# Kernel tuning notes

Measured on AMD Instinct MI355X. Metric: run time of the kernel, lower is better.

Reference implementation:

```python
import jax, jax.numpy as jnp
import numpy as np
from jax import lax

B, N = 2, 8192
H = W = 256
KNN_K = 33          # includes self, as in _computeDensity
RADIUS = 0.1
CUTOFF = 1.0        # cutOffThreshold: a dx^2 + b dy^2 + c dx dy <= cutoffC
WIN = 9             # fixed splat footprint (ellipse extents ~1-3 px, clamped at 15 in source)
EPS = 1e-8


def setup_inputs() -> dict:
    key = jax.random.key(0)
    k1, k2, k3, k4, k5 = jax.random.split(key, 5)
    points = jax.random.normal(k1, (B, N, 3), jnp.float32)
    # projected pixel coordinates, kept a few px inside the image
    proj_xy = jax.random.uniform(k2, (B, N, 2), jnp.float32, 4.0, W - 4.0)
    # ellipse coefficients a, b, c with 4ab - c^2 > 0 (valid ellipse)
    ab = jax.random.uniform(k3, (B, N, 2), jnp.float32, 0.1, 0.5)
    c = jax.random.uniform(k4, (B, N, 1), jnp.float32, -0.05, 0.05)
    ellipse_params = jnp.concatenate([ab, c], axis=-1)
    colors = jax.random.uniform(k5, (B, N, 3), jnp.float32)
    return {"points": points, "proj_xy": proj_xy,
            "ellipse_params": ellipse_params, "colors": colors}


def _compute_density(points):
    # faithful jax version of _computeDensity: KNN gaussian density
    r2 = RADIUS * RADIUS
    sq = jnp.sum(points * points, axis=-1)                      # [B,N]
    # pairwise squared distances [B,N,N]
    d2 = sq[:, :, None] + sq[:, None, :] - 2.0 * jnp.einsum('bnd,bmd->bnm', points, points)
    neg_d2k, _ = lax.top_k(-d2, KNN_K)                          # k nearest (incl. self)
    d2k = jnp.maximum(-neg_d2k[:, :, 1:], 0.0)                  # drop self, [B,N,K-1]
    w = jnp.exp(-d2k / r2 / 4.0)
    w = jnp.where(d2k > r2, 0.0, w)
    return jnp.sum(w, axis=-1)                                  # [B,N]


def reference(points, proj_xy, ellipse_params, colors):
    density = _compute_density(points)                          # [B,N]
    a = ellipse_params[..., 0]
    b = ellipse_params[..., 1]
    c = ellipse_params[..., 2]
    x = proj_xy[..., 0]
    y = proj_xy[..., 1]
    # _findEllipseBoundingBox extents, clamped at 15 as in the grad path
    den = 4.0 * a * b - c * c
    xE = jnp.minimum(jnp.sqrt(4.0 * b * CUTOFF / den), 15.0)    # [B,N]
    yE = jnp.minimum(jnp.sqrt(4.0 * a * CUTOFF / den), 15.0)

    # fixed WINxWIN footprint around floor(proj) (jit-friendly bbox)
    R = WIN // 2
    offs = jnp.arange(-R, R + 1, dtype=jnp.float32)
    ox, oy = jnp.meshgrid(offs, offs, indexing='ij')
    ox = ox.reshape(-1)                                         # [P]
    oy = oy.reshape(-1)
    x0 = jnp.floor(x)
    y0 = jnp.floor(y)
    px = x0[..., None] + ox                                     # [B,N,P]
    py = y0[..., None] + oy
    dx = px - x[..., None]
    dy = py - y[..., None]
    # elliptical gaussian splat weight, truncated at cutoff
    Q = a[..., None] * dx * dx + b[..., None] * dy * dy + c[..., None] * dx * dy
    inb = (px >= 0) & (px < W) & (py >= 0) & (py < H)
    bbox = (jnp.abs(dx) <= xE[..., None] + 1.0) & (jnp.abs(dy) <= yE[..., None] + 1.0)
    mask = inb & bbox & (Q <= CUTOFF)
    w = jnp.where(mask, jnp.exp(-0.5 * Q) * density[..., None], 0.0)  # [B,N,P]

    # scatter-accumulate weighted colors and weights per pixel
    pxi = jnp.clip(px.astype(jnp.int32), 0, W - 1)
    pyi = jnp.clip(py.astype(jnp.int32), 0, H - 1)
    bi = jnp.arange(B, dtype=jnp.int32)[:, None, None]
    flat = ((bi * H + pyi) * W + pxi).reshape(-1)               # [B*N*P]
    wc = (w[..., None] * colors[:, :, None, :]).reshape(-1, 3)
    wf = w.reshape(-1)
    img_c = jnp.zeros((B * H * W, 3), jnp.float32).at[flat].add(wc)
    img_w = jnp.zeros((B * H * W,), jnp.float32).at[flat].add(wf)
    image = img_c / (img_w[:, None] + EPS)
    return image.reshape(B, H, W, 3)
```

## Files before the change

### kernel.cpp

```cpp
#include <hip/hip_runtime.h>

#define NB  2
#define NP  8192
#define IMH 256
#define IMW 256
#define NBKT 1024

constexpr float R2F = 0.01f;
constexpr float BK_SCALE = 64.f;
constexpr float BK_OFF   = 8.f;
#define BK_PAD 7

__device__ __forceinline__ int bucket_of(float x) {
    int b = (int)floorf((x + BK_OFF) * BK_SCALE);
    return min(max(b, 0), NBKT - 1);
}

__global__ __launch_bounds__(1024) void binsort_kernel(
    const float* __restrict__ pts, float4* __restrict__ sorted,
    int* __restrict__ sidx, int* __restrict__ offsets)
{
    __shared__ int cntA[NBKT], cntB[NBKT], cur[NBKT];
    const int b   = blockIdx.x;
    const int tid = threadIdx.x;
    const float* __restrict__ base = pts + (size_t)b * NP * 3;

    cntA[tid] = 0;
    __syncthreads();

    float xs[8], ys[8], zs[8]; int bks[8];
    #pragma unroll
    for (int k = 0; k < 8; ++k) {
        const int i = k * 1024 + tid;
        xs[k] = base[i * 3 + 0];
        ys[k] = base[i * 3 + 1];
        zs[k] = base[i * 3 + 2];
        bks[k] = bucket_of(xs[k]);
        atomicAdd(&cntA[bks[k]], 1);
    }
    __syncthreads();

    int* src = cntA; int* dst = cntB;
    for (int off = 1; off < NBKT; off <<= 1) {
        int v = src[tid];
        if (tid >= off) v += src[tid - off];
        dst[tid] = v;
        __syncthreads();
        int* tmp = src; src = dst; dst = tmp;
    }
    const int start = (tid == 0) ? 0 : src[tid - 1];
    offsets[b * (NBKT + 1) + tid] = start;
    if (tid == 0) offsets[b * (NBKT + 1) + NBKT] = NP;
    cur[tid] = start;
    __syncthreads();

    #pragma unroll
    for (int k = 0; k < 8; ++k) {
        const int i = k * 1024 + tid;
        const int slot = atomicAdd(&cur[bks[k]], 1);
        const float sq = __fadd_rn(__fadd_rn(__fmul_rn(xs[k], xs[k]),
                                             __fmul_rn(ys[k], ys[k])),
                                   __fmul_rn(zs[k], zs[k]));
        sorted[(size_t)b * NP + slot] = make_float4(xs[k], ys[k], zs[k], sq);
        sidx  [(size_t)b * NP + slot] = i;
    }
}

__global__ __launch_bounds__(256) void density_kernel(
    const float4* __restrict__ sorted, const int* __restrict__ sidx,
    const int* __restrict__ offsets, float* __restrict__ density)
{
    const int wave = threadIdx.x >> 6, lane = threadIdx.x & 63;
    const int w  = blockIdx.x * 4 + wave;
    const int s0 = w * 8;
    const int b  = s0 >> 13;
    const int sb = s0 & (NP - 1);
    const float4* __restrict__ sp = sorted + (size_t)b * NP;

    float xi[8], yi[8], zi[8], sqi[8], sum[8];
    #pragma unroll
    for (int t = 0; t < 8; ++t) {
        const float4 p = sp[sb + t];
        xi[t] = p.x; yi[t] = p.y; zi[t] = p.z; sqi[t] = p.w;
        sum[t] = 0.f;
    }
    const int blo = max(bucket_of(xi[0]) - BK_PAD, 0);
    const int bhi = min(bucket_of(xi[7]) + BK_PAD + 1, NBKT);
    const int jlo = offsets[b * (NBKT + 1) + blo];
    const int jhi = offsets[b * (NBKT + 1) + bhi];

    for (int jj = jlo + lane; jj < jhi; jj += 64) {
        const float4 pj = sp[jj];
        #pragma unroll
        for (int t = 0; t < 8; ++t) {
            const float dot = __fmaf_rn(zi[t], pj.z,
                              __fmaf_rn(yi[t], pj.y,
                              __fmul_rn(xi[t], pj.x)));
            const float d2 = __fsub_rn(__fadd_rn(sqi[t], pj.w),
                                       __fadd_rn(dot, dot));
            const float d2c = fmaxf(d2, 0.f);
            if (jj != sb + t && d2c <= R2F)
                sum[t] += expf(__fmul_rn(__fdiv_rn(d2c, R2F), -0.25f));
        }
    }
    #pragma unroll
    for (int t = 0; t < 8; ++t) {
        float s = sum[t];
        #pragma unroll
        for (int off2 = 32; off2; off2 >>= 1) s += __shfl_down(s, off2, 64);
        if (lane == 0) density[(size_t)b * NP + sidx[(size_t)b * NP + sb + t]] = s;
    }
}

__global__ __launch_bounds__(256) void splat_kernel(
    const float* __restrict__ proj, const float* __restrict__ ell,
    const float* __restrict__ cols, const float* __restrict__ density,
    float* __restrict__ img_c, float* __restrict__ img_w)
{
    const int wave = threadIdx.x >> 6;
    const int lane = threadIdx.x & 63;
    const int pid  = blockIdx.x * 4 + wave;
    const float dens = density[pid];
    if (dens == 0.f) return;
    const int b = pid >> 13;
    const float x = proj[pid * 2 + 0], y = proj[pid * 2 + 1];
    const float a  = ell[pid * 3 + 0], bb = ell[pid * 3 + 1], c = ell[pid * 3 + 2];
    const float cr = cols[pid * 3 + 0], cg = cols[pid * 3 + 1], cb = cols[pid * 3 + 2];

    const float den = __fsub_rn(__fmul_rn(__fmul_rn(4.f, a), bb),
                                __fmul_rn(c, c));
    const float xE = fminf(__fsqrt_rn(__fdiv_rn(__fmul_rn(4.f, bb), den)), 15.f);
    const float yE = fminf(__fsqrt_rn(__fdiv_rn(__fmul_rn(4.f, a),  den)), 15.f);
    const float xEp1 = __fadd_rn(xE, 1.f);
    const float yEp1 = __fadd_rn(yE, 1.f);
    const float x0 = floorf(x), y0 = floorf(y);

    for (int idx = lane; idx < 81; idx += 64) {
        const float ox = (float)(idx / 9) - 4.f;
        const float oy = (float)(idx % 9) - 4.f;
        const float px = __fadd_rn(x0, ox);
        const float py = __fadd_rn(y0, oy);
        if (px < 0.f || px >= 256.f || py < 0.f || py >= 256.f) continue;
        const float dx = __fsub_rn(px, x);
        const float dy = __fsub_rn(py, y);
        if (fabsf(dx) > xEp1 || fabsf(dy) > yEp1) continue;
        const float Q = __fadd_rn(__fadd_rn(__fmul_rn(__fmul_rn(a, dx), dx),
                                            __fmul_rn(__fmul_rn(bb, dy), dy)),
                                  __fmul_rn(__fmul_rn(c, dx), dy));
        if (!(Q <= 1.0f)) continue;
        const float w = __fmul_rn(expf(__fmul_rn(-0.5f, Q)), dens);
        const int pxi = (int)px, pyi = (int)py;
        const int flat = ((b << 8) + pyi) * IMW + pxi;
        atomicAdd(&img_c[flat * 3 + 0], __fmul_rn(w, cr));
        atomicAdd(&img_c[flat * 3 + 1], __fmul_rn(w, cg));
        atomicAdd(&img_c[flat * 3 + 2], __fmul_rn(w, cb));
        atomicAdd(&img_w[flat],         w);
    }
}

__global__ void norm_kernel(float* __restrict__ out, const float* __restrict__ img_w)
{
    const int p = blockIdx.x * 256 + threadIdx.x;
    if (p < NB * IMH * IMW) {
        const float d = __fadd_rn(img_w[p], 1e-8f);
        out[3 * p + 0] = __fdiv_rn(out[3 * p + 0], d);
        out[3 * p + 1] = __fdiv_rn(out[3 * p + 1], d);
        out[3 * p + 2] = __fdiv_rn(out[3 * p + 2], d);
    }
}

extern "C" void kernel_launch(void* const* d_in, const int* in_sizes, int n_in,
                              void* d_out, int out_size, void* d_ws, size_t ws_size,
                              hipStream_t stream)
{
    const float* points = (const float*)d_in[0];
    const float* proj   = (const float*)d_in[1];
    const float* ell    = (const float*)d_in[2];
    const float* cols   = (const float*)d_in[3];
    float* out = (float*)d_out;

    float4* sorted  = (float4*)d_ws;
    float*  img_w   = (float*)(sorted + (size_t)NB * NP);
    float*  density = img_w + (size_t)NB * IMH * IMW;
    int*    sidx    = (int*)(density + (size_t)NB * NP);
    int*    offsets = sidx + (size_t)NB * NP;

    hipMemsetAsync(d_out, 0, sizeof(float) * (size_t)out_size, stream);
    hipMemsetAsync(img_w, 0, sizeof(float) * (size_t)NB * IMH * IMW, stream);

    binsort_kernel<<<NB, 1024, 0, stream>>>(points, sorted, sidx, offsets);
    density_kernel<<<NB * NP / 32, 256, 0, stream>>>(sorted, sidx, offsets, density);
    splat_kernel  <<<NB * NP / 4,  256, 0, stream>>>(proj, ell, cols, density, out, img_w);
    norm_kernel   <<<(NB * IMH * IMW + 255) / 256, 256, 0, stream>>>(out, img_w);
}
```

Before: 47.43 us.

## Split two-block bin sort into grid-wide histogram, scan and scatter kernels

Replaces the single-block-per-batch bin sort with three kernels: a grid-wide global-atomic histogram, a per-batch scan, and a grid-wide scatter using global atomic cursors. The two memsets are also replaced by a single zeroing kernel that clears the output, the weight image and the histogram. The goal is to stop running the sort on only two CUs and to drop the memset calls. In exchange it adds kernel launches, contended global atomics on the histogram buckets, and a nondeterministic order within each bucket.

After: 49.06 us. 1.03x slower.

```diff
diff --git a/kernel.cpp b/kernel.cpp
--- a/kernel.cpp
+++ b/kernel.cpp
@@ -16,31 +16,33 @@
     return min(max(b, 0), NBKT - 1);
 }
 
-__global__ __launch_bounds__(1024) void binsort_kernel(
-    const float* __restrict__ pts, float4* __restrict__ sorted,
-    int* __restrict__ sidx, int* __restrict__ offsets)
-{
-    __shared__ int cntA[NBKT], cntB[NBKT], cur[NBKT];
-    const int b   = blockIdx.x;
-    const int tid = threadIdx.x;
-    const float* __restrict__ base = pts + (size_t)b * NP * 3;
-
-    cntA[tid] = 0;
+__global__ __launch_bounds__(256) void init_kernel(
+    float4* __restrict__ out4, float4* __restrict__ imgw4, int4* __restrict__ gh4)
+{
+    const int t = blockIdx.x * 256 + threadIdx.x;
+    const float4 z4 = make_float4(0.f, 0.f, 0.f, 0.f);
+    if (t < 98304) out4[t] = z4;
+    if (t < 32768) imgw4[t] = z4;
+    if (t < 512)   gh4[t]   = make_int4(0, 0, 0, 0);
+}
+
+__global__ __launch_bounds__(256) void hist_kernel(
+    const float* __restrict__ pts, int* __restrict__ ghist)
+{
+    const int tid = blockIdx.x * 256 + threadIdx.x;
+    const int b = tid >> 13;
+    const float x = pts[(size_t)tid * 3];
+    atomicAdd(&ghist[b * NBKT + bucket_of(x)], 1);
+}
+
+__global__ __launch_bounds__(1024) void scan_kernel(
+    const int* __restrict__ ghist, int* __restrict__ offsets, int* __restrict__ gcur)
+{
+    __shared__ int A[NBKT], Bs[NBKT];
+    const int b = blockIdx.x, tid = threadIdx.x;
+    A[tid] = ghist[b * NBKT + tid];
     __syncthreads();
-
-    float xs[8], ys[8], zs[8]; int bks[8];
-    #pragma unroll
-    for (int k = 0; k < 8; ++k) {
-        const int i = k * 1024 + tid;
-        xs[k] = base[i * 3 + 0];
-        ys[k] = base[i * 3 + 1];
-        zs[k] = base[i * 3 + 2];
-        bks[k] = bucket_of(xs[k]);
-        atomicAdd(&cntA[bks[k]], 1);
-    }
-    __syncthreads();
-
-    int* src = cntA; int* dst = cntB;
+    int* src = A; int* dst = Bs;
     for (int off = 1; off < NBKT; off <<= 1) {
         int v = src[tid];
         if (tid >= off) v += src[tid - off];
@@ -48,22 +50,26 @@
         __syncthreads();
         int* tmp = src; src = dst; dst = tmp;
     }
-    const int start = (tid == 0) ? 0 : src[tid - 1];
+    const int start = tid ? src[tid - 1] : 0;
     offsets[b * (NBKT + 1) + tid] = start;
+    gcur[b * NBKT + tid] = start;
     if (tid == 0) offsets[b * (NBKT + 1) + NBKT] = NP;
-    cur[tid] = start;
-    __syncthreads();
-
-    #pragma unroll
-    for (int k = 0; k < 8; ++k) {
-        const int i = k * 1024 + tid;
-        const int slot = atomicAdd(&cur[bks[k]], 1);
-        const float sq = __fadd_rn(__fadd_rn(__fmul_rn(xs[k], xs[k]),
-                                             __fmul_rn(ys[k], ys[k])),
-                                   __fmul_rn(zs[k], zs[k]));
-        sorted[(size_t)b * NP + slot] = make_float4(xs[k], ys[k], zs[k], sq);
-        sidx  [(size_t)b * NP + slot] = i;
-    }
+}
+
+__global__ __launch_bounds__(256) void scatter_kernel(
+    const float* __restrict__ pts, int* __restrict__ gcur,
+    float4* __restrict__ sorted, int* __restrict__ sidx)
+{
+    const int tid = blockIdx.x * 256 + threadIdx.x;
+    const int b = tid >> 13, i = tid & (NP - 1);
+    const float x = pts[(size_t)tid * 3 + 0];
+    const float y = pts[(size_t)tid * 3 + 1];
+    const float z = pts[(size_t)tid * 3 + 2];
+    const int slot = atomicAdd(&gcur[b * NBKT + bucket_of(x)], 1);
+    const float sq = __fadd_rn(__fadd_rn(__fmul_rn(x, x), __fmul_rn(y, y)),
+                               __fmul_rn(z, z));
+    sorted[(size_t)b * NP + slot] = make_float4(x, y, z, sq);
+    sidx  [(size_t)b * NP + slot] = i;
 }
 
 __global__ __launch_bounds__(256) void density_kernel(
@@ -184,11 +190,14 @@
     float*  density = img_w + (size_t)NB * IMH * IMW;
     int*    sidx    = (int*)(density + (size_t)NB * NP);
     int*    offsets = sidx + (size_t)NB * NP;
-
-    hipMemsetAsync(d_out, 0, sizeof(float) * (size_t)out_size, stream);
-    hipMemsetAsync(img_w, 0, sizeof(float) * (size_t)NB * IMH * IMW, stream);
-
-    binsort_kernel<<<NB, 1024, 0, stream>>>(points, sorted, sidx, offsets);
+    int*    ghist   = offsets + NB * (NBKT + 1) + 3;
+    ghist = (int*)((((size_t)(offsets + NB * (NBKT + 1))) + 15) & ~(size_t)15);
+    int*    gcur    = ghist + NB * NBKT;
+
+    init_kernel   <<<384, 256, 0, stream>>>((float4*)out, (float4*)img_w, (int4*)ghist);
+    hist_kernel   <<<NB * NP / 256, 256, 0, stream>>>(points, ghist);
+    scan_kernel   <<<NB, 1024, 0, stream>>>(ghist, offsets, gcur);
+    scatter_kernel<<<NB * NP / 256, 256, 0, stream>>>(points, gcur, sorted, sidx);
     density_kernel<<<NB * NP / 32, 256, 0, stream>>>(sorted, sidx, offsets, density);
     splat_kernel  <<<NB * NP / 4,  256, 0, stream>>>(proj, ell, cols, density, out, img_w);
     norm_kernel   <<<(NB * IMH * IMW + 255) / 256, 256, 0, stream>>>(out, img_w);
```

## Fuse density and splat kernels; replace memsets with one zero-init kernel

Applied to the files above, without the earlier changes.

The density kernel now splats each point right after reducing its density, using the sorted-to-original index to fetch projection, ellipse and color data, so the separate splat kernel and the density buffer round trip go away. The two hipMemsetAsync calls are replaced by one custom kernel that zeroes the output and weight images with float4 stores. This removes a kernel launch and the memset overheads. In exchange, each wave splats 8 points serially after its density loop, and it reads proj/ell/cols through scattered sorted indices.

Measured after the change: 41.25 us. -13.0%, faster.

```diff
diff --git a/kernel.cpp b/kernel.cpp
--- a/kernel.cpp
+++ b/kernel.cpp
@@ -14,6 +14,15 @@
 __device__ __forceinline__ int bucket_of(float x) {
     int b = (int)floorf((x + BK_OFF) * BK_SCALE);
     return min(max(b, 0), NBKT - 1);
+}
+
+__global__ __launch_bounds__(256) void init_kernel(
+    float4* __restrict__ out4, float4* __restrict__ imgw4)
+{
+    const int t = blockIdx.x * 256 + threadIdx.x;
+    const float4 z4 = make_float4(0.f, 0.f, 0.f, 0.f);
+    if (t < 98304) out4[t] = z4;
+    if (t < 32768) imgw4[t] = z4;
 }
 
 __global__ __launch_bounds__(1024) void binsort_kernel(
@@ -66,9 +75,12 @@
     }
 }
 
-__global__ __launch_bounds__(256) void density_kernel(
+__global__ __launch_bounds__(256) void densplat_kernel(
     const float4* __restrict__ sorted, const int* __restrict__ sidx,
-    const int* __restrict__ offsets, float* __restrict__ density)
+    const int* __restrict__ offsets,
+    const float* __restrict__ proj, const float* __restrict__ ell,
+    const float* __restrict__ cols,
+    float* __restrict__ img_c, float* __restrict__ img_w)
 {
     const int wave = threadIdx.x >> 6, lane = threadIdx.x & 63;
     const int w  = blockIdx.x * 4 + wave;
@@ -103,58 +115,49 @@
                 sum[t] += expf(__fmul_rn(__fdiv_rn(d2c, R2F), -0.25f));
         }
     }
+
     #pragma unroll
     for (int t = 0; t < 8; ++t) {
         float s = sum[t];
         #pragma unroll
         for (int off2 = 32; off2; off2 >>= 1) s += __shfl_down(s, off2, 64);
-        if (lane == 0) density[(size_t)b * NP + sidx[(size_t)b * NP + sb + t]] = s;
-    }
-}
+        const float dens = __shfl(s, 0, 64);
+        if (dens == 0.f) continue;
 
-__global__ __launch_bounds__(256) void splat_kernel(
-    const float* __restrict__ proj, const float* __restrict__ ell,
-    const float* __restrict__ cols, const float* __restrict__ density,
-    float* __restrict__ img_c, float* __restrict__ img_w)
-{
-    const int wave = threadIdx.x >> 6;
-    const int lane = threadIdx.x & 63;
-    const int pid  = blockIdx.x * 4 + wave;
-    const float dens = density[pid];
-    if (dens == 0.f) return;
-    const int b = pid >> 13;
-    const float x = proj[pid * 2 + 0], y = proj[pid * 2 + 1];
-    const float a  = ell[pid * 3 + 0], bb = ell[pid * 3 + 1], c = ell[pid * 3 + 2];
-    const float cr = cols[pid * 3 + 0], cg = cols[pid * 3 + 1], cb = cols[pid * 3 + 2];
+        const size_t gp = (size_t)b * NP + sidx[(size_t)b * NP + sb + t];
+        const float x = proj[gp * 2 + 0], y = proj[gp * 2 + 1];
+        const float a  = ell[gp * 3 + 0], bb = ell[gp * 3 + 1], c = ell[gp * 3 + 2];
+        const float cr = cols[gp * 3 + 0], cg = cols[gp * 3 + 1], cb = cols[gp * 3 + 2];
 
-    const float den = __fsub_rn(__fmul_rn(__fmul_rn(4.f, a), bb),
-                                __fmul_rn(c, c));
-    const float xE = fminf(__fsqrt_rn(__fdiv_rn(__fmul_rn(4.f, bb), den)), 15.f);
-    const float yE = fminf(__fsqrt_rn(__fdiv_rn(__fmul_rn(4.f, a),  den)), 15.f);
-    const float xEp1 = __fadd_rn(xE, 1.f);
-    const float yEp1 = __fadd_rn(yE, 1.f);
-    const float x0 = floorf(x), y0 = floorf(y);
+        const float den = __fsub_rn(__fmul_rn(__fmul_rn(4.f, a), bb),
+                                    __fmul_rn(c, c));
+        const float xE = fminf(__fsqrt_rn(__fdiv_rn(__fmul_rn(4.f, bb), den)), 15.f);
+        const float yE = fminf(__fsqrt_rn(__fdiv_rn(__fmul_rn(4.f, a),  den)), 15.f);
+        const float xEp1 = __fadd_rn(xE, 1.f);
+        const float yEp1 = __fadd_rn(yE, 1.f);
+        const float x0 = floorf(x), y0 = floorf(y);
 
-    for (int idx = lane; idx < 81; idx += 64) {
-        const float ox = (float)(idx / 9) - 4.f;
-        const float oy = (float)(idx % 9) - 4.f;
-        const float px = __fadd_rn(x0, ox);
-        const float py = __fadd_rn(y0, oy);
-        if (px < 0.f || px >= 256.f || py < 0.f || py >= 256.f) continue;
-        const float dx = __fsub_rn(px, x);
-        const float dy = __fsub_rn(py, y);
-        if (fabsf(dx) > xEp1 || fabsf(dy) > yEp1) continue;
-        const float Q = __fadd_rn(__fadd_rn(__fmul_rn(__fmul_rn(a, dx), dx),
-                                            __fmul_rn(__fmul_rn(bb, dy), dy)),
-                                  __fmul_rn(__fmul_rn(c, dx), dy));
-        if (!(Q <= 1.0f)) continue;
-        const float w = __fmul_rn(expf(__fmul_rn(-0.5f, Q)), dens);
-        const int pxi = (int)px, pyi = (int)py;
-        const int flat = ((b << 8) + pyi) * IMW + pxi;
-        atomicAdd(&img_c[flat * 3 + 0], __fmul_rn(w, cr));
-        atomicAdd(&img_c[flat * 3 + 1], __fmul_rn(w, cg));
-        atomicAdd(&img_c[flat * 3 + 2], __fmul_rn(w, cb));
-        atomicAdd(&img_w[flat],         w);
+        for (int idx = lane; idx < 81; idx += 64) {
+            const float ox = (float)(idx / 9) - 4.f;
+            const float oy = (float)(idx % 9) - 4.f;
+            const float px = __fadd_rn(x0, ox);
+            const float py = __fadd_rn(y0, oy);
+            if (px < 0.f || px >= 256.f || py < 0.f || py >= 256.f) continue;
+            const float dx = __fsub_rn(px, x);
+            const float dy = __fsub_rn(py, y);
+            if (fabsf(dx) > xEp1 || fabsf(dy) > yEp1) continue;
+            const float Q = __fadd_rn(__fadd_rn(__fmul_rn(__fmul_rn(a, dx), dx),
+                                                __fmul_rn(__fmul_rn(bb, dy), dy)),
+                                      __fmul_rn(__fmul_rn(c, dx), dy));
+            if (!(Q <= 1.0f)) continue;
+            const float wgt = __fmul_rn(expf(__fmul_rn(-0.5f, Q)), dens);
+            const int pxi = (int)px, pyi = (int)py;
+            const int flat = ((b << 8) + pyi) * IMW + pxi;
+            atomicAdd(&img_c[flat * 3 + 0], __fmul_rn(wgt, cr));
+            atomicAdd(&img_c[flat * 3 + 1], __fmul_rn(wgt, cg));
+            atomicAdd(&img_c[flat * 3 + 2], __fmul_rn(wgt, cb));
+            atomicAdd(&img_w[flat],         wgt);
+        }
     }
 }
 
@@ -181,15 +184,12 @@
 
     float4* sorted  = (float4*)d_ws;
     float*  img_w   = (float*)(sorted + (size_t)NB * NP);
-    float*  density = img_w + (size_t)NB * IMH * IMW;
-    int*    sidx    = (int*)(density + (size_t)NB * NP);
+    int*    sidx    = (int*)(img_w + (size_t)NB * IMH * IMW);
     int*    offsets = sidx + (size_t)NB * NP;
 
-    hipMemsetAsync(d_out, 0, sizeof(float) * (size_t)out_size, stream);
-    hipMemsetAsync(img_w, 0, sizeof(float) * (size_t)NB * IMH * IMW, stream);
-
-    binsort_kernel<<<NB, 1024, 0, stream>>>(points, sorted, sidx, offsets);
-    density_kernel<<<NB * NP / 32, 256, 0, stream>>>(sorted, sidx, offsets, density);
-    splat_kernel  <<<NB * NP / 4,  256, 0, stream>>>(proj, ell, cols, density, out, img_w);
-    norm_kernel   <<<(NB * IMH * IMW + 255) / 256, 256, 0, stream>>>(out, img_w);
+    init_kernel    <<<384, 256, 0, stream>>>((float4*)out, (float4*)img_w);
+    binsort_kernel <<<NB, 1024, 0, stream>>>(points, sorted, sidx, offsets);
+    densplat_kernel<<<NB * NP / 32, 256, 0, stream>>>(sorted, sidx, offsets,
+                                                      proj, ell, cols, out, img_w);
+    norm_kernel    <<<(NB * IMH * IMW + 255) / 256, 256, 0, stream>>>(out, img_w);
 }
```
